# Performance work log

Measured on AMD Instinct MI355X. Metric: run time of the kernel, lower is better.

Reference implementation:

```python
import jax, jax.numpy as jnp
import numpy as np

D_MODEL = 1024
N_HEADS = 16
D_K = D_MODEL // N_HEADS
B = 2048
S = 20  # hardcoded by the 20x20 decay matrix in the original module


def setup_inputs() -> dict:
    key = jax.random.key(0)
    ks = jax.random.split(key, 8)
    bound = np.sqrt(6.0 / (D_MODEL + D_MODEL))  # xavier_uniform gain=1
    lin_b = 1.0 / np.sqrt(D_MODEL)              # default torch Linear bias init
    Q = jax.random.normal(ks[0], (B, S, D_MODEL), dtype=jnp.float32)
    W_Q = jax.random.uniform(ks[1], (D_MODEL, D_MODEL), jnp.float32, -bound, bound)
    W_K = jax.random.uniform(ks[2], (D_MODEL, D_MODEL), jnp.float32, -bound, bound)
    W_V = jax.random.uniform(ks[3], (D_MODEL, D_MODEL), jnp.float32, -bound, bound)
    b_Q = jax.random.uniform(ks[4], (D_MODEL,), jnp.float32, -lin_b, lin_b)
    b_K = jax.random.uniform(ks[5], (D_MODEL,), jnp.float32, -lin_b, lin_b)
    b_V = jax.random.uniform(ks[6], (D_MODEL,), jnp.float32, -lin_b, lin_b)
    length = jax.random.randint(ks[7], (B,), 1, S + 1, dtype=jnp.int64)
    return {"Q": Q, "W_Q": W_Q, "b_Q": b_Q, "W_K": W_K, "b_K": b_K,
            "W_V": W_V, "b_V": b_V, "length": length}


def reference(Q, W_Q, b_Q, W_K, b_K, W_V, b_V, length):
    # torch Linear: y = x @ W.T + b
    def proj(x, W, b):
        y = x @ W.T + b                              # [B,S,D]
        return y.reshape(B, S, N_HEADS, D_K).transpose(0, 2, 1, 3)  # [B,H,S,dk]

    q = proj(Q, W_Q, b_Q)
    k = proj(Q, W_K, b_K)
    v = proj(Q, W_V, b_V)

    scores = jnp.einsum('bhqd,bhkd->bhqk', q, k) / np.sqrt(D_K)
    scores = jnp.exp(scores)                         # exp normalization, NO max-subtract (faithful)
    # key-side mask: arange(S) < length, broadcast over heads and query dim
    mask = (jnp.arange(S)[None, :] < length[:, None]).astype(scores.dtype)  # [B,S]
    scores = scores * mask[:, None, None, :]
    attn = scores / (jnp.sum(scores, axis=-1, keepdims=True) + 1e-8)
    context = jnp.einsum('bhqk,bhkd->bhqd', attn, v)

    # decay matrix Md[i,j] = -(|i-j|)
    idx = jnp.arange(S)
    Md = -jnp.abs(idx[:, None] - idx[None, :]).astype(context.dtype)  # [S,S]
    deAtt = context + jnp.einsum('qk,bhkd->bhqd', Md, v)

    out = deAtt.transpose(0, 2, 1, 3).reshape(B, S, D_MODEL)
    return out
```

## Files before the change

kernel.cpp:

```cpp
#include <hip/hip_runtime.h>

typedef unsigned short u16;
typedef __attribute__((ext_vector_type(8))) __bf16 bf16x8;
typedef __attribute__((ext_vector_type(4))) float f32x4;
typedef __attribute__((ext_vector_type(16))) float f32x16;

__device__ __forceinline__ u16 f2bf(float x) {
    union { float f; unsigned int u; } v; v.f = x;
    unsigned int r = v.u + 0x7fffu + ((v.u >> 16) & 1u);
    return (u16)(r >> 16);
}
__device__ __forceinline__ unsigned int pack2bf(float a, float b) {
    return (unsigned int)f2bf(a) | ((unsigned int)f2bf(b) << 16);
}

typedef const __attribute__((address_space(1))) void* gas_ptr;
typedef __attribute__((address_space(3))) void* las_ptr;
#define GLOAD_LDS16(g, l) __builtin_amdgcn_global_load_lds((gas_ptr)(const void*)(g), (las_ptr)(void*)(l), 16, 0, 0)

__global__ void cvt_bf16(const float* __restrict__ src, u16* __restrict__ dst, int n8) {
    int i = blockIdx.x * blockDim.x + threadIdx.x;
    if (i >= n8) return;
    const float4* s = (const float4*)src + (size_t)i * 2;
    float4 a = s[0], b = s[1];
    union { u16 u[8]; uint4 v; } o;
    o.u[0] = f2bf(a.x); o.u[1] = f2bf(a.y); o.u[2] = f2bf(a.z); o.u[3] = f2bf(a.w);
    o.u[4] = f2bf(b.x); o.u[5] = f2bf(b.y); o.u[6] = f2bf(b.z); o.u[7] = f2bf(b.w);
    *((uint4*)dst + i) = o.v;
}

__global__ __launch_bounds__(512, 2) void gemm_qkv(
    const u16* __restrict__ X, const u16* __restrict__ W,
    const float* __restrict__ bQ, const float* __restrict__ bK,
    const float* __restrict__ bV, u16* __restrict__ Y)
{
    __shared__ __align__(16) u16 AB[2][2][16384];
    const int tid = threadIdx.x;
    const int w = tid >> 6, lane = tid & 63;
    const int wave_m = w >> 2, wave_n = w & 3;
    const int l15 = lane & 15, l4 = lane >> 4, l7 = lane & 7;

    const int nwg = gridDim.x;
    const int bid = blockIdx.x;
    const int q = nwg >> 3, r = nwg & 7;
    const int xcd = bid & 7, idx = bid >> 3;
    const int swz = (xcd < r ? xcd * (q + 1) : r * (q + 1) + (xcd - r) * q) + idx;
    const int bx = swz % 12, by = swz / 12;
    const size_t mBase = (size_t)by << 8;
    const int nBase = bx << 8;

    const int lr = lane >> 3, lc = lane & 7, lcs = lc ^ lr;
    const u16* gA = X + (mBase + (size_t)(w * 32 + lr)) * 1024 + lcs * 8;
    const u16* gB = W + ((size_t)(nBase + w * 32 + lr)) * 1024 + lcs * 8;
    const int stOff = (w * 32) * 64;

    f32x4 acc[8][4];
#pragma unroll
    for (int mi = 0; mi < 8; ++mi)
#pragma unroll
        for (int ni = 0; ni < 4; ++ni)
#pragma unroll
            for (int rr = 0; rr < 4; ++rr) acc[mi][ni][rr] = 0.f;

#pragma unroll
    for (int j = 0; j < 4; ++j) {
        GLOAD_LDS16(gA + j * 8192, &AB[0][0][stOff + j * 512]);
        GLOAD_LDS16(gB + j * 8192, &AB[0][1][stOff + j * 512]);
    }
    asm volatile("s_waitcnt vmcnt(0)" ::: "memory");
    __builtin_amdgcn_s_barrier();
    __builtin_amdgcn_sched_barrier(0);

    const int aR = wave_m * 128 + l15;
    const int bR = wave_n * 64 + l15;
    const int ck0 = (l4 ^ l7) * 8;
    const int ck1 = ((4 | l4) ^ l7) * 8;

    for (int t = 0; t < 16; ++t) {
        u16* curA = (t & 1) ? &AB[1][0][0] : &AB[0][0][0];
        u16* curB = (t & 1) ? &AB[1][1][0] : &AB[0][1][0];
        u16* stA  = (t & 1) ? &AB[0][0][stOff] : &AB[1][0][stOff];
        u16* stB  = (t & 1) ? &AB[0][1][stOff] : &AB[1][1][stOff];
        const int kNxt = (t + 1) * 64;
        const bool pf = (t < 15);

        bf16x8 a[4], b[4];
#pragma unroll
        for (int ni = 0; ni < 4; ++ni)
            b[ni] = *(const bf16x8*)&curB[(bR + ni * 16) * 64 + ck0];
#pragma unroll
        for (int mi = 0; mi < 4; ++mi)
            a[mi] = *(const bf16x8*)&curA[(aR + mi * 16) * 64 + ck0];
        if (pf) {
            GLOAD_LDS16(gA + kNxt,        stA);
            GLOAD_LDS16(gA + kNxt + 8192, stA + 512);
            GLOAD_LDS16(gB + kNxt,        stB);
            GLOAD_LDS16(gB + kNxt + 8192, stB + 512);
        }
        __builtin_amdgcn_s_barrier();
        __builtin_amdgcn_s_setprio(1);
#pragma unroll
        for (int mi = 0; mi < 4; ++mi)
#pragma unroll
            for (int ni = 0; ni < 4; ++ni)
                acc[mi][ni] = __builtin_amdgcn_mfma_f32_16x16x32_bf16(a[mi], b[ni], acc[mi][ni], 0, 0, 0);
        __builtin_amdgcn_s_setprio(0);
        __builtin_amdgcn_s_barrier();

#pragma unroll
        for (int mi = 0; mi < 4; ++mi)
            a[mi] = *(const bf16x8*)&curA[(aR + (mi + 4) * 16) * 64 + ck0];
        if (pf) {
            GLOAD_LDS16(gA + kNxt + 16384, stA + 1024);
            GLOAD_LDS16(gA + kNxt + 24576, stA + 1536);
            GLOAD_LDS16(gB + kNxt + 16384, stB + 1024);
            GLOAD_LDS16(gB + kNxt + 24576, stB + 1536);
        }
        __builtin_amdgcn_s_barrier();
        __builtin_amdgcn_s_setprio(1);
#pragma unroll
        for (int mi = 0; mi < 4; ++mi)
#pragma unroll
            for (int ni = 0; ni < 4; ++ni)
                acc[mi + 4][ni] = __builtin_amdgcn_mfma_f32_16x16x32_bf16(a[mi], b[ni], acc[mi + 4][ni], 0, 0, 0);
        __builtin_amdgcn_s_setprio(0);
        __builtin_amdgcn_s_barrier();

#pragma unroll
        for (int ni = 0; ni < 4; ++ni)
            b[ni] = *(const bf16x8*)&curB[(bR + ni * 16) * 64 + ck1];
#pragma unroll
        for (int mi = 0; mi < 4; ++mi)
            a[mi] = *(const bf16x8*)&curA[(aR + mi * 16) * 64 + ck1];
        __builtin_amdgcn_s_barrier();
        __builtin_amdgcn_s_setprio(1);
#pragma unroll
        for (int mi = 0; mi < 4; ++mi)
#pragma unroll
            for (int ni = 0; ni < 4; ++ni)
                acc[mi][ni] = __builtin_amdgcn_mfma_f32_16x16x32_bf16(a[mi], b[ni], acc[mi][ni], 0, 0, 0);
        __builtin_amdgcn_s_setprio(0);
        __builtin_amdgcn_s_barrier();

#pragma unroll
        for (int mi = 0; mi < 4; ++mi)
            a[mi] = *(const bf16x8*)&curA[(aR + (mi + 4) * 16) * 64 + ck1];
        __builtin_amdgcn_s_barrier();
        __builtin_amdgcn_s_setprio(1);
#pragma unroll
        for (int mi = 0; mi < 4; ++mi)
#pragma unroll
            for (int ni = 0; ni < 4; ++ni)
                acc[mi + 4][ni] = __builtin_amdgcn_mfma_f32_16x16x32_bf16(a[mi], b[ni], acc[mi + 4][ni], 0, 0, 0);
        __builtin_amdgcn_s_setprio(0);
        asm volatile("s_waitcnt vmcnt(0)" ::: "memory");
        __builtin_amdgcn_s_barrier();
        __builtin_amdgcn_sched_barrier(0);
    }

    const int third = nBase >> 10;
    const float* bias = (third == 0) ? bQ : ((third == 1) ? bK : bV);
    const int bcol = (nBase & 1023) + wave_n * 64 + l15;
    float bv[4];
#pragma unroll
    for (int ni = 0; ni < 4; ++ni) bv[ni] = bias[bcol + ni * 16];
#pragma unroll
    for (int mi = 0; mi < 8; ++mi) {
        size_t rb = mBase + wave_m * 128 + mi * 16 + l4 * 4;
#pragma unroll
        for (int ni = 0; ni < 4; ++ni) {
            int col = nBase + wave_n * 64 + ni * 16 + l15;
#pragma unroll
            for (int rr = 0; rr < 4; ++rr)
                Y[(rb + rr) * 3072 + col] = f2bf(acc[mi][ni][rr] + bv[ni]);
        }
    }
}

__global__ __launch_bounds__(256) void attn_dec(
    const u16* __restrict__ Y, const int* __restrict__ lenp, float* __restrict__ out)
{
    __shared__ __align__(16) u16 vLds[4][1280];
    const int tid = threadIdx.x;
    const int w = tid >> 6, lane = tid & 63;
    const int u = blockIdx.x * 4 + w;
    const int b = u >> 4, h = u & 15;
    const int L = lenp[b];
    const int i32 = lane & 31, hw = lane >> 5;
    const int m19 = (i32 < 19) ? i32 : 19;

    const u16* qb = Y + (size_t)b * 61440 + h * 64;
    const u16* kb = qb + 1024;
    const u16* vb = qb + 2048;

    uint4 vReg[3];
    int vC[3];
#pragma unroll
    for (int t = 0; t < 3; ++t) {
        int c = t * 64 + lane;
        vC[t] = c;
        if (c < 160)
            vReg[t] = *(const uint4*)(vb + (size_t)(c >> 3) * 3072 + (c & 7) * 8);
    }

    f32x16 s;
    for (int r = 0; r < 16; ++r) s[r] = 0.f;
#pragma unroll
    for (int kc = 0; kc < 4; ++kc) {
        const int off = kc * 16 + hw * 8;
        bf16x8 ak = *(const bf16x8*)(kb + (size_t)m19 * 3072 + off);
        bf16x8 bq = *(const bf16x8*)(qb + (size_t)m19 * 3072 + off);
        s = __builtin_amdgcn_mfma_f32_32x32x16_bf16(ak, bq, s, 0, 0, 0);
    }

#pragma unroll
    for (int t = 0; t < 3; ++t)
        if (vC[t] < 160) *(uint4*)&vLds[w][vC[t] * 8] = vReg[t];

    float ev[16];
    float part = 0.f;
#pragma unroll
    for (int r = 0; r < 16; ++r) {
        int j = (r & 3) + ((r >> 2) << 3) + (hw << 2);
        float e = (i32 < 20 && j < L) ? __expf(s[r] * 0.125f) : 0.f;
        ev[r] = e;
        part += e;
    }
    float sum = part + __shfl_xor(part, 32, 64);
    float inv = 1.f / (sum + 1e-8f);

    unsigned int wOwn[8];
#pragma unroll
    for (int p = 0; p < 8; ++p) {
        float c01[2];
#pragma unroll
        for (int q2 = 0; q2 < 2; ++q2) {
            int r = 2 * p + q2;
            int j = (r & 3) + ((r >> 2) << 3) + (hw << 2);
            float c = ev[r] * inv;
            if (i32 < 20 && j < 20)
                c -= (float)((i32 > j) ? (i32 - j) : (j - i32));
            else
                c = 0.f;
            c01[q2] = c;
        }
        wOwn[p] = pack2bf(c01[0], c01[1]);
    }
    unsigned int wPar[8];
#pragma unroll
    for (int p = 0; p < 8; ++p)
        wPar[p] = (unsigned int)__shfl_xor((int)wOwn[p], 32, 64);

    union { unsigned int u[4]; bf16x8 v; } A0, A1;
    if (hw == 0) {
        A0.u[0] = wOwn[0]; A0.u[1] = wOwn[1]; A0.u[2] = wPar[0]; A0.u[3] = wPar[1];
        A1.u[0] = wOwn[4]; A1.u[1] = wOwn[5]; A1.u[2] = wPar[4]; A1.u[3] = wPar[5];
    } else {
        A0.u[0] = wPar[2]; A0.u[1] = wPar[3]; A0.u[2] = wOwn[2]; A0.u[3] = wOwn[3];
        A1.u[0] = wPar[6]; A1.u[1] = wPar[7]; A1.u[2] = wOwn[6]; A1.u[3] = wOwn[7];
    }

    f32x16 o0, o1;
    for (int r = 0; r < 16; ++r) { o0[r] = 0.f; o1[r] = 0.f; }
#pragma unroll
    for (int kc = 0; kc < 2; ++kc) {
        bf16x8 ac = (kc == 0) ? A0.v : A1.v;
        bf16x8 bv0, bv1;
#pragma unroll
        for (int jj = 0; jj < 8; ++jj) {
            int j = kc * 16 + hw * 8 + jj;
            int jc = (j < 19) ? j : 19;
            bv0[jj] = *(const __bf16*)&vLds[w][jc * 64 + i32];
            bv1[jj] = *(const __bf16*)&vLds[w][jc * 64 + 32 + i32];
        }
        o0 = __builtin_amdgcn_mfma_f32_32x32x16_bf16(ac, bv0, o0, 0, 0, 0);
        o1 = __builtin_amdgcn_mfma_f32_32x32x16_bf16(ac, bv1, o1, 0, 0, 0);
    }

#pragma unroll
    for (int r = 0; r < 16; ++r) {
        int i = (r & 3) + ((r >> 2) << 3) + (hw << 2);
        if (i < 20) {
            size_t ro = ((size_t)b * 20 + i) * 1024 + h * 64 + i32;
            out[ro] = o0[r];
            out[ro + 32] = o1[r];
        }
    }
}

extern "C" void kernel_launch(void* const* d_in, const int* in_sizes, int n_in,
                              void* d_out, int out_size, void* d_ws, size_t ws_size,
                              hipStream_t stream) {
    const float* Q   = (const float*)d_in[0];
    const float* W_Q = (const float*)d_in[1];
    const float* b_Q = (const float*)d_in[2];
    const float* W_K = (const float*)d_in[3];
    const float* b_K = (const float*)d_in[4];
    const float* W_V = (const float*)d_in[5];
    const float* b_V = (const float*)d_in[6];
    const int*   len = (const int*)d_in[7];
    float* out = (float*)d_out;

    int NB = 2048;
    while (NB > 64 && 6291456ull + (unsigned long long)NB * 163840ull > (unsigned long long)ws_size)
        NB >>= 1;
    if (6291456ull + (unsigned long long)NB * 163840ull > (unsigned long long)ws_size)
        return;

    u16* Wbf = (u16*)d_ws;
    u16* Xbf = Wbf + 3145728;
    u16* Yq  = Xbf + (size_t)NB * 20480;

    cvt_bf16<<<512, 256, 0, stream>>>(W_Q, Wbf,           131072);
    cvt_bf16<<<512, 256, 0, stream>>>(W_K, Wbf + 1048576, 131072);
    cvt_bf16<<<512, 256, 0, stream>>>(W_V, Wbf + 2097152, 131072);

    const int nsl = 2048 / NB;
    for (int sI = 0; sI < nsl; ++sI) {
        int bBase = sI * NB;
        cvt_bf16<<<NB * 10, 256, 0, stream>>>(Q + (size_t)bBase * 20480, Xbf, NB * 2560);
        int nwg = 12 * ((NB * 20) >> 8);
        gemm_qkv<<<nwg, 512, 0, stream>>>(Xbf, Wbf, b_Q, b_K, b_V, Yq);
        attn_dec<<<NB * 4, 256, 0, stream>>>(Yq, len + bBase, out + (size_t)bBase * 20480);
    }
}
```

Baseline: 636.5 us.

## Shrink QKV GEMM tile to 128x256 and use triple-buffered LDS prefetch

The QKV projection GEMM drops its M tile from 256 to 128 rows, which doubles the workgroup count and halves the accumulator registers per wave. The LDS staging moves from double to triple buffering with a rotating pointer set, so loads run two K-steps ahead and the per-iteration wait becomes vmcnt(6) instead of a full drain. The aim is to hide global-load latency and improve occupancy. The cost is less reuse of each loaded B tile (more W traffic per FLOP), 144 KB of LDS per workgroup, and fewer MFMAs between barriers.

New measurement: 665.8 us. 4.6% more time.

```diff
diff --git a/kernel.cpp b/kernel.cpp
--- a/kernel.cpp
+++ b/kernel.cpp
@@ -34,7 +34,7 @@
     const float* __restrict__ bQ, const float* __restrict__ bK,
     const float* __restrict__ bV, u16* __restrict__ Y)
 {
-    __shared__ __align__(16) u16 AB[2][2][16384];
+    __shared__ __align__(16) u16 S[73728];
     const int tid = threadIdx.x;
     const int w = tid >> 6, lane = tid & 63;
     const int wave_m = w >> 2, wave_n = w & 3;
@@ -46,56 +46,59 @@
     const int xcd = bid & 7, idx = bid >> 3;
     const int swz = (xcd < r ? xcd * (q + 1) : r * (q + 1) + (xcd - r) * q) + idx;
     const int bx = swz % 12, by = swz / 12;
-    const size_t mBase = (size_t)by << 8;
+    const size_t mBase = (size_t)by << 7;
     const int nBase = bx << 8;
 
     const int lr = lane >> 3, lc = lane & 7, lcs = lc ^ lr;
-    const u16* gA = X + (mBase + (size_t)(w * 32 + lr)) * 1024 + lcs * 8;
+    const u16* gA = X + (mBase + (size_t)(w * 16 + lr)) * 1024 + lcs * 8;
     const u16* gB = W + ((size_t)(nBase + w * 32 + lr)) * 1024 + lcs * 8;
-    const int stOff = (w * 32) * 64;
-
-    f32x4 acc[8][4];
-#pragma unroll
-    for (int mi = 0; mi < 8; ++mi)
+    const int stA = w * 1024;
+    const int stB = 8192 + w * 2048;
+
+    f32x4 acc[4][4];
+#pragma unroll
+    for (int mi = 0; mi < 4; ++mi)
 #pragma unroll
         for (int ni = 0; ni < 4; ++ni)
 #pragma unroll
             for (int rr = 0; rr < 4; ++rr) acc[mi][ni][rr] = 0.f;
 
-#pragma unroll
-    for (int j = 0; j < 4; ++j) {
-        GLOAD_LDS16(gA + j * 8192, &AB[0][0][stOff + j * 512]);
-        GLOAD_LDS16(gB + j * 8192, &AB[0][1][stOff + j * 512]);
-    }
-    asm volatile("s_waitcnt vmcnt(0)" ::: "memory");
+    u16* bc = S;
+    u16* bn = S + 24576;
+    u16* bs = S + 49152;
+
+#pragma unroll
+    for (int l = 0; l < 2; ++l) GLOAD_LDS16(gA + l * 8192,      bc + stA + l * 512);
+#pragma unroll
+    for (int l = 0; l < 4; ++l) GLOAD_LDS16(gB + l * 8192,      bc + stB + l * 512);
+#pragma unroll
+    for (int l = 0; l < 2; ++l) GLOAD_LDS16(gA + l * 8192 + 64, bn + stA + l * 512);
+#pragma unroll
+    for (int l = 0; l < 4; ++l) GLOAD_LDS16(gB + l * 8192 + 64, bn + stB + l * 512);
+    asm volatile("s_waitcnt vmcnt(6)" ::: "memory");
     __builtin_amdgcn_s_barrier();
     __builtin_amdgcn_sched_barrier(0);
 
-    const int aR = wave_m * 128 + l15;
-    const int bR = wave_n * 64 + l15;
+    const int aRb = wave_m * 64 + l15;
+    const int bRb = wave_n * 64 + l15;
     const int ck0 = (l4 ^ l7) * 8;
     const int ck1 = ((4 | l4) ^ l7) * 8;
 
     for (int t = 0; t < 16; ++t) {
-        u16* curA = (t & 1) ? &AB[1][0][0] : &AB[0][0][0];
-        u16* curB = (t & 1) ? &AB[1][1][0] : &AB[0][1][0];
-        u16* stA  = (t & 1) ? &AB[0][0][stOff] : &AB[1][0][stOff];
-        u16* stB  = (t & 1) ? &AB[0][1][stOff] : &AB[1][1][stOff];
-        const int kNxt = (t + 1) * 64;
-        const bool pf = (t < 15);
-
+        const int kNxt = (t + 2) * 64;
+        const bool pf = (t < 14);
         bf16x8 a[4], b[4];
+
+#pragma unroll
+        for (int mi = 0; mi < 4; ++mi)
+            a[mi] = *(const bf16x8*)&bc[(aRb + mi * 16) * 64 + ck0];
 #pragma unroll
         for (int ni = 0; ni < 4; ++ni)
-            b[ni] = *(const bf16x8*)&curB[(bR + ni * 16) * 64 + ck0];
-#pragma unroll
-        for (int mi = 0; mi < 4; ++mi)
-            a[mi] = *(const bf16x8*)&curA[(aR + mi * 16) * 64 + ck0];
+            b[ni] = *(const bf16x8*)&bc[8192 + (bRb + ni * 16) * 64 + ck0];
         if (pf) {
-            GLOAD_LDS16(gA + kNxt,        stA);
-            GLOAD_LDS16(gA + kNxt + 8192, stA + 512);
-            GLOAD_LDS16(gB + kNxt,        stB);
-            GLOAD_LDS16(gB + kNxt + 8192, stB + 512);
+            GLOAD_LDS16(gA + kNxt,         bs + stA);
+            GLOAD_LDS16(gA + kNxt + 8192,  bs + stA + 512);
+            GLOAD_LDS16(gB + kNxt,         bs + stB);
         }
         __builtin_amdgcn_s_barrier();
         __builtin_amdgcn_s_setprio(1);
@@ -109,29 +112,15 @@
 
 #pragma unroll
         for (int mi = 0; mi < 4; ++mi)
-            a[mi] = *(const bf16x8*)&curA[(aR + (mi + 4) * 16) * 64 + ck0];
+            a[mi] = *(const bf16x8*)&bc[(aRb + mi * 16) * 64 + ck1];
+#pragma unroll
+        for (int ni = 0; ni < 4; ++ni)
+            b[ni] = *(const bf16x8*)&bc[8192 + (bRb + ni * 16) * 64 + ck1];
         if (pf) {
-            GLOAD_LDS16(gA + kNxt + 16384, stA + 1024);
-            GLOAD_LDS16(gA + kNxt + 24576, stA + 1536);
-            GLOAD_LDS16(gB + kNxt + 16384, stB + 1024);
-            GLOAD_LDS16(gB + kNxt + 24576, stB + 1536);
-        }
-        __builtin_amdgcn_s_barrier();
-        __builtin_amdgcn_s_setprio(1);
-#pragma unroll
-        for (int mi = 0; mi < 4; ++mi)
-#pragma unroll
-            for (int ni = 0; ni < 4; ++ni)
-                acc[mi + 4][ni] = __builtin_amdgcn_mfma_f32_16x16x32_bf16(a[mi], b[ni], acc[mi + 4][ni], 0, 0, 0);
-        __builtin_amdgcn_s_setprio(0);
-        __builtin_amdgcn_s_barrier();
-
-#pragma unroll
-        for (int ni = 0; ni < 4; ++ni)
-            b[ni] = *(const bf16x8*)&curB[(bR + ni * 16) * 64 + ck1];
-#pragma unroll
-        for (int mi = 0; mi < 4; ++mi)
-            a[mi] = *(const bf16x8*)&curA[(aR + mi * 16) * 64 + ck1];
+            GLOAD_LDS16(gB + kNxt + 8192,  bs + stB + 512);
+            GLOAD_LDS16(gB + kNxt + 16384, bs + stB + 1024);
+            GLOAD_LDS16(gB + kNxt + 24576, bs + stB + 1536);
+        }
         __builtin_amdgcn_s_barrier();
         __builtin_amdgcn_s_setprio(1);
 #pragma unroll
@@ -140,22 +129,11 @@
             for (int ni = 0; ni < 4; ++ni)
                 acc[mi][ni] = __builtin_amdgcn_mfma_f32_16x16x32_bf16(a[mi], b[ni], acc[mi][ni], 0, 0, 0);
         __builtin_amdgcn_s_setprio(0);
-        __builtin_amdgcn_s_barrier();
-
-#pragma unroll
-        for (int mi = 0; mi < 4; ++mi)
-            a[mi] = *(const bf16x8*)&curA[(aR + (mi + 4) * 16) * 64 + ck1];
-        __builtin_amdgcn_s_barrier();
-        __builtin_amdgcn_s_setprio(1);
-#pragma unroll
-        for (int mi = 0; mi < 4; ++mi)
-#pragma unroll
-            for (int ni = 0; ni < 4; ++ni)
-                acc[mi + 4][ni] = __builtin_amdgcn_mfma_f32_16x16x32_bf16(a[mi], b[ni], acc[mi + 4][ni], 0, 0, 0);
-        __builtin_amdgcn_s_setprio(0);
-        asm volatile("s_waitcnt vmcnt(0)" ::: "memory");
+        if (pf) asm volatile("s_waitcnt vmcnt(6)" ::: "memory");
+        else    asm volatile("s_waitcnt vmcnt(0)" ::: "memory");
         __builtin_amdgcn_s_barrier();
         __builtin_amdgcn_sched_barrier(0);
+        u16* tmp = bc; bc = bn; bn = bs; bs = tmp;
     }
 
     const int third = nBase >> 10;
@@ -165,8 +143,8 @@
 #pragma unroll
     for (int ni = 0; ni < 4; ++ni) bv[ni] = bias[bcol + ni * 16];
 #pragma unroll
-    for (int mi = 0; mi < 8; ++mi) {
-        size_t rb = mBase + wave_m * 128 + mi * 16 + l4 * 4;
+    for (int mi = 0; mi < 4; ++mi) {
+        size_t rb = mBase + wave_m * 64 + mi * 16 + l4 * 4;
 #pragma unroll
         for (int ni = 0; ni < 4; ++ni) {
             int col = nBase + wave_n * 64 + ni * 16 + l15;
@@ -319,7 +297,7 @@
     for (int sI = 0; sI < nsl; ++sI) {
         int bBase = sI * NB;
         cvt_bf16<<<NB * 10, 256, 0, stream>>>(Q + (size_t)bBase * 20480, Xbf, NB * 2560);
-        int nwg = 12 * ((NB * 20) >> 8);
+        int nwg = 12 * ((NB * 20) >> 7);
         gemm_qkv<<<nwg, 512, 0, stream>>>(Xbf, Wbf, b_Q, b_K, b_V, Yq);
         attn_dec<<<NB * 4, 256, 0, stream>>>(Yq, len + bBase, out + (size_t)bBase * 20480);
     }
```
